# Performance work log

Measured on AMD Instinct MI355X. Metric: run time of the kernel, lower is better.

The kernel has to match this reference:

```python
import jax, jax.numpy as jnp
import numpy as np

B, NA, NT, P, DA, DM, H = 1, 4096, 1024, 32768, 128, 512, 4
DH = DA // H
DF = 4 * DA
WINDOW = 16


def _layer_norm(x, g=None, b=None, eps=1e-5):
    m = jnp.mean(x, axis=-1, keepdims=True)
    v = jnp.var(x, axis=-1, keepdims=True)
    xn = (x - m) / jnp.sqrt(v + eps)
    if g is not None:
        xn = xn * g + b
    return xn


def setup_inputs() -> dict:
    key = jax.random.key(0)
    ks = jax.random.split(key, 32)
    r = lambda k, s: (jax.random.normal(k, s, dtype=jnp.float32) * 0.05)
    return {
        'q': r(ks[0], (B, NA, DA)),
        'c_atom': r(ks[1], (B, NA, DA)),
        'h_cond': r(ks[2], (B, NT, DM)),
        'p_lm': r(ks[3], (B, P, 16)),
        't_emb': r(ks[4], (B, DA)),
        'cond_proj_w': r(ks[5], (DM, DA)), 'cond_proj_b': r(ks[6], (DA,)),
        'adaln1_w': r(ks[7], (DA, 2 * DA)), 'adaln1_b': r(ks[8], (2 * DA,)),
        'adaln2_w': r(ks[9], (DA, 2 * DA)), 'adaln2_b': r(ks[10], (2 * DA,)),
        'ln_g': jnp.ones((DA,), jnp.float32), 'ln_b': jnp.zeros((DA,), jnp.float32),
        'wq': r(ks[11], (DA, DA)), 'wk': r(ks[12], (DA, DA)),
        'wv': r(ks[13], (DA, DA)), 'wg': r(ks[14], (DA, DA)),
        'wo': r(ks[15], (DA, DA)),
        'pair_w': r(ks[16], (16, H)), 'pair_b': r(ks[17], (H,)),
        'gate1_w': r(ks[18], (DA, DA)), 'gate1_b': r(ks[19], (DA,)),
        'gate2_w': r(ks[20], (DA, DA)), 'gate2_b': r(ks[21], (DA,)),
        'sw1': r(ks[22], (DA, DF)), 'sw3': r(ks[23], (DA, DF)),
        'sw2': r(ks[24], (DF, DA)),
        'p_lm_idx': jax.random.randint(ks[25], (B, P, 2), 0, NA, dtype=jnp.int32),
        'token_idx': jnp.sort(jax.random.randint(ks[26], (B, NA), 0, NT, dtype=jnp.int32), axis=-1),
    }


def _forward(q, c_atom, h_cond, p_lm, t_emb,
             cond_proj_w, cond_proj_b, adaln1_w, adaln1_b, adaln2_w, adaln2_b,
             ln_g, ln_b, wq, wk, wv, wg, wo, pair_w, pair_b,
             gate1_w, gate1_b, gate2_w, gate2_b, sw1, sw3, sw2,
             p_lm_idx, token_idx):
    Bq, N, D = q.shape
    # gather token conditioning to atoms: (B, NA, DM)
    h_atoms = jax.vmap(lambda h, t: h[t])(h_cond, token_idx)
    cond = t_emb[:, None, :] + h_atoms @ cond_proj_w + cond_proj_b  # (B, NA, DA)
    g1, b1 = jnp.split(cond @ adaln1_w + adaln1_b, 2, axis=-1)
    q_n = (1.0 + g1) * _layer_norm(q, ln_g, ln_b) + b1

    Q = (q_n @ wq).reshape(Bq, N, H, DH)
    K = (q_n @ wk).reshape(Bq, N, H, DH)
    V = (q_n @ wv).reshape(Bq, N, H, DH)
    G_flat = q_n @ wg  # (B, N, DA); permute/reshape in torch is identity on layout

    scores = jnp.einsum('bihd,bjhd->bhij', Q, K) / jnp.sqrt(jnp.float32(DH))

    # scattered pair bias: (B, P, H) -> dense (B, H, N, N)
    bias = p_lm @ pair_w + pair_b  # (B, P, H)

    def scat(idx, bb):
        return jnp.zeros((N, N, H), bb.dtype).at[idx[:, 0], idx[:, 1]].set(bb)

    pair_bias = jax.vmap(scat)(p_lm_idx, bias).transpose(0, 3, 1, 2)
    scores = scores + pair_bias

    pos = jnp.arange(N)
    window = jnp.abs(pos[:, None] - pos[None, :]) <= WINDOW  # (N, N)
    scores = jnp.where(window[None, None, :, :], scores, -jnp.inf)

    attn = jax.nn.softmax(scores, axis=-1)
    att_out = jnp.einsum('bhij,bjhd->bihd', attn, V).reshape(Bq, N, D)

    q1 = q + jax.nn.sigmoid(G_flat) * (att_out @ wo)
    q1 = q1 + jax.nn.sigmoid(c_atom @ gate1_w + gate1_b) * q1

    g2, b2 = jnp.split(cond @ adaln2_w + adaln2_b, 2, axis=-1)
    q_n2 = (1.0 + g2) * _layer_norm(q1) + b2
    swi = (jax.nn.silu(q_n2 @ sw1) * (q_n2 @ sw3)) @ sw2
    q2 = q1 + jax.nn.sigmoid(c_atom @ gate2_w + gate2_b) * swi
    return q2  # atom_pad_mask is all-ones -> final mask multiply is identity


def reference(q, c_atom, h_cond, p_lm, t_emb,
              cond_proj_w, cond_proj_b, adaln1_w, adaln1_b, adaln2_w, adaln2_b,
              ln_g, ln_b, wq, wk, wv, wg, wo, pair_w, pair_b,
              gate1_w, gate1_b, gate2_w, gate2_b, sw1, sw3, sw2,
              p_lm_idx, token_idx):
    return _forward(q, c_atom, h_cond, p_lm, t_emb,
                    cond_proj_w, cond_proj_b, adaln1_w, adaln1_b, adaln2_w, adaln2_b,
                    ln_g, ln_b, wq, wk, wv, wg, wo, pair_w, pair_b,
                    gate1_w, gate1_b, gate2_w, gate2_b, sw1, sw3, sw2,
                    p_lm_idx, token_idx)
```

## Files before the change

### kernel.cpp

```cpp
#include <hip/hip_runtime.h>
#include <math.h>

#define NA   4096
#define DA   128
#define DM   512
#define NT   1024
#define HH   4
#define DF   512
#define PP   32768
#define WIN  16
#define BAND 33
#define KSTR 132

typedef __attribute__((ext_vector_type(8))) short bf16x8;
typedef __attribute__((ext_vector_type(4))) float f32x4;

__device__ __forceinline__ float sigmoidf_(float x) { return 1.0f / (1.0f + __expf(-x)); }
__device__ __forceinline__ ushort f2bf(float f) {
    union { float f; unsigned int i; } x; x.f = f;
    unsigned int r = x.i + 0x7fffu + ((x.i >> 16) & 1u);
    return (ushort)(r >> 16);
}

__global__ __launch_bounds__(256) void k_prep(
    const float* __restrict__ hc, const float* __restrict__ ca,
    const float* __restrict__ cw, const float* __restrict__ a1, const float* __restrict__ a2,
    const float* __restrict__ wq, const float* __restrict__ wk, const float* __restrict__ wv,
    const float* __restrict__ wg, const float* __restrict__ wo,
    const float* __restrict__ g1, const float* __restrict__ g2,
    const float* __restrict__ s1, const float* __restrict__ s3, const float* __restrict__ s2,
    ushort* hcb, ushort* cab, ushort* cwT, ushort* a1T, ushort* a2T,
    ushort* wqT, ushort* wkT, ushort* wvT, ushort* wgT, ushort* woT,
    ushort* g1T, ushort* g2T, ushort* s1T, ushort* s3T, ushort* s2T,
    float* band)
{
    __shared__ float tile[32][33];
    const int y = blockIdx.y, bx = blockIdx.x, tid = threadIdx.x;
    if (y <= 1) {
        const float4* src = (const float4*)(y == 0 ? hc : ca);
        ushort* dst = y == 0 ? hcb : cab;
        for (int i = bx * 256 + tid; i < 131072; i += 16384) {
            float4 v = src[i];
            ushort4 st; st.x = f2bf(v.x); st.y = f2bf(v.y); st.z = f2bf(v.z); st.w = f2bf(v.w);
            *(ushort4*)&dst[(size_t)i * 4] = st;
        }
        return;
    }
    if (y == 15) {
        float4 z = {0.f, 0.f, 0.f, 0.f};
        float4* b4 = (float4*)band;
        for (int i = bx * 256 + tid; i < 135168; i += 16384) b4[i] = z;
        return;
    }
    const float* src; ushort* dst; int K, N;
    switch (y) {
        case 2:  src = cw; dst = cwT; K = 512; N = 128; break;
        case 3:  src = a1; dst = a1T; K = 128; N = 256; break;
        case 4:  src = a2; dst = a2T; K = 128; N = 256; break;
        case 5:  src = wq; dst = wqT; K = 128; N = 128; break;
        case 6:  src = wk; dst = wkT; K = 128; N = 128; break;
        case 7:  src = wv; dst = wvT; K = 128; N = 128; break;
        case 8:  src = wg; dst = wgT; K = 128; N = 128; break;
        case 9:  src = wo; dst = woT; K = 128; N = 128; break;
        case 10: src = g1; dst = g1T; K = 128; N = 128; break;
        case 11: src = g2; dst = g2T; K = 128; N = 128; break;
        case 12: src = s1; dst = s1T; K = 128; N = 512; break;
        case 13: src = s3; dst = s3T; K = 128; N = 512; break;
        default: src = s2; dst = s2T; K = 512; N = 128; break;
    }
    const int tn_cnt = N >> 5;
    if (bx >= (K >> 5) * tn_cnt) return;
    const int k0 = (bx / tn_cnt) << 5, n0 = (bx % tn_cnt) << 5;
    {
        int r = tid >> 3, c = (tid & 7) << 2;
        float4 v = *(const float4*)&src[(size_t)(k0 + r) * N + n0 + c];
        tile[r][c + 0] = v.x; tile[r][c + 1] = v.y;
        tile[r][c + 2] = v.z; tile[r][c + 3] = v.w;
    }
    __syncthreads();
    {
        int rn = tid >> 3, ck = (tid & 7) << 2;
        ushort4 st;
        st.x = f2bf(tile[ck + 0][rn]);
        st.y = f2bf(tile[ck + 1][rn]);
        st.z = f2bf(tile[ck + 2][rn]);
        st.w = f2bf(tile[ck + 3][rn]);
        *(ushort4*)&dst[(size_t)(n0 + rn) * K + k0 + ck] = st;
    }
}

__global__ __launch_bounds__(256) void k_condmod(
    const ushort* __restrict__ hcb, const int* __restrict__ tok,
    const ushort* __restrict__ cwT, const float* __restrict__ t_emb,
    const float* __restrict__ cond_b, const ushort* __restrict__ cab,
    const ushort* __restrict__ a1T, const ushort* __restrict__ a2T,
    const ushort* __restrict__ g1T, const ushort* __restrict__ g2T,
    const float* __restrict__ ad1b, const float* __restrict__ ad2b,
    const float* __restrict__ g1b, const float* __restrict__ g2b,
    const float* __restrict__ p_lm, const float* __restrict__ pair_w,
    const float* __restrict__ pair_b, const int* __restrict__ p_idx,
    float* __restrict__ band,
    float* __restrict__ gb1, float* __restrict__ gb2,
    float* __restrict__ gate1, float* __restrict__ gate2)
{
    const int tid = threadIdx.x, b = blockIdx.x;
    if (b >= 256) {
        int p = (b - 256) * 256 + tid;
        int i = p_idx[2 * p], j = p_idx[2 * p + 1];
        int d = j - i + WIN;
        if (d < 0 || d > 2 * WIN) return;
        float v0 = pair_b[0], v1 = pair_b[1], v2 = pair_b[2], v3 = pair_b[3];
        #pragma unroll
        for (int k = 0; k < 16; ++k) {
            float a = p_lm[p * 16 + k];
            v0 = fmaf(a, pair_w[k * 4 + 0], v0);
            v1 = fmaf(a, pair_w[k * 4 + 1], v1);
            v2 = fmaf(a, pair_w[k * 4 + 2], v2);
            v3 = fmaf(a, pair_w[k * 4 + 3], v3);
        }
        size_t base = ((size_t)i * HH) * BAND + d;
        band[base + 0 * BAND] = v0;
        band[base + 1 * BAND] = v1;
        band[base + 2 * BAND] = v2;
        band[base + 3 * BAND] = v3;
        return;
    }
    __shared__ ushort cond_s[16 * 128];
    const int l = tid & 63, wv = tid >> 6;
    const int cl = l & 15, kq = l >> 4, ko = kq * 8;
    const int r0 = b * 16;
    {
        const int n0 = wv * 32;
        const ushort* Arow = hcb + (size_t)tok[r0 + cl] * DM;
        const ushort* Wc = cwT + (size_t)(n0 + cl) * DM;
        f32x4 acc[2] = {};
        #pragma unroll
        for (int ks = 0; ks < 16; ++ks) {
            bf16x8 a = *(const bf16x8*)(Arow + ks * 32 + ko);
            #pragma unroll
            for (int nf = 0; nf < 2; ++nf) {
                bf16x8 bb = *(const bf16x8*)(Wc + (size_t)nf * 16 * DM + ks * 32 + ko);
                acc[nf] = __builtin_amdgcn_mfma_f32_16x16x32_bf16(a, bb, acc[nf], 0, 0, 0);
            }
        }
        #pragma unroll
        for (int nf = 0; nf < 2; ++nf) {
            int col = n0 + nf * 16 + cl;
            float add = t_emb[col] + cond_b[col];
            #pragma unroll
            for (int r = 0; r < 4; ++r) {
                int row = kq * 4 + r;
                int byte = row * 256 + col * 2;
                byte ^= (row & 7) << 4;
                *(ushort*)((char*)cond_s + byte) = f2bf(acc[nf][r] + add);
            }
        }
    }
    __syncthreads();
    {
        const int n0 = wv * 64;
        const ushort* W1c = a1T + (size_t)(n0 + cl) * DA;
        const ushort* W2c = a2T + (size_t)(n0 + cl) * DA;
        f32x4 acc1[4] = {}, acc2[4] = {};
        #pragma unroll
        for (int ks = 0; ks < 4; ++ks) {
            int byteA = cl * 256 + (ks * 32 + ko) * 2;
            byteA ^= (cl & 7) << 4;
            bf16x8 a = *(const bf16x8*)((char*)cond_s + byteA);
            #pragma unroll
            for (int nf = 0; nf < 4; ++nf) {
                bf16x8 b1 = *(const bf16x8*)(W1c + (size_t)nf * 16 * DA + ks * 32 + ko);
                acc1[nf] = __builtin_amdgcn_mfma_f32_16x16x32_bf16(a, b1, acc1[nf], 0, 0, 0);
                bf16x8 b2 = *(const bf16x8*)(W2c + (size_t)nf * 16 * DA + ks * 32 + ko);
                acc2[nf] = __builtin_amdgcn_mfma_f32_16x16x32_bf16(a, b2, acc2[nf], 0, 0, 0);
            }
        }
        #pragma unroll
        for (int nf = 0; nf < 4; ++nf) {
            int col = n0 + nf * 16 + cl;
            float b1v = ad1b[col], b2v = ad2b[col];
            #pragma unroll
            for (int r = 0; r < 4; ++r) {
                size_t rc = (size_t)(r0 + kq * 4 + r) * 256 + col;
                gb1[rc] = acc1[nf][r] + b1v;
                gb2[rc] = acc2[nf][r] + b2v;
            }
        }
    }
    {
        const int n0 = wv * 32;
        const ushort* Arow = cab + (size_t)(r0 + cl) * DA;
        const ushort* W1c = g1T + (size_t)(n0 + cl) * DA;
        const ushort* W2c = g2T + (size_t)(n0 + cl) * DA;
        f32x4 acc1[2] = {}, acc2[2] = {};
        #pragma unroll
        for (int ks = 0; ks < 4; ++ks) {
            bf16x8 a = *(const bf16x8*)(Arow + ks * 32 + ko);
            #pragma unroll
            for (int nf = 0; nf < 2; ++nf) {
                bf16x8 b1 = *(const bf16x8*)(W1c + (size_t)nf * 16 * DA + ks * 32 + ko);
                acc1[nf] = __builtin_amdgcn_mfma_f32_16x16x32_bf16(a, b1, acc1[nf], 0, 0, 0);
                bf16x8 b2 = *(const bf16x8*)(W2c + (size_t)nf * 16 * DA + ks * 32 + ko);
                acc2[nf] = __builtin_amdgcn_mfma_f32_16x16x32_bf16(a, b2, acc2[nf], 0, 0, 0);
            }
        }
        #pragma unroll
        for (int nf = 0; nf < 2; ++nf) {
            int col = n0 + nf * 16 + cl;
            float b1v = g1b[col], b2v = g2b[col];
            #pragma unroll
            for (int r = 0; r < 4; ++r) {
                size_t rc = (size_t)(r0 + kq * 4 + r) * DA + col;
                gate1[rc] = sigmoidf_(acc1[nf][r] + b1v);
                gate2[rc] = sigmoidf_(acc2[nf][r] + b2v);
            }
        }
    }
}

__global__ __launch_bounds__(512) void k_mega(
    const float* __restrict__ qg, const float* __restrict__ gb1,
    const float* __restrict__ gb2, const float* __restrict__ gate1,
    const float* __restrict__ gate2, const float* __restrict__ ln_g,
    const float* __restrict__ ln_b, const float* __restrict__ band,
    const ushort* __restrict__ wqT, const ushort* __restrict__ wkT,
    const ushort* __restrict__ wvT, const ushort* __restrict__ wgT,
    const ushort* __restrict__ woT, const ushort* __restrict__ s1T,
    const ushort* __restrict__ s3T, const ushort* __restrict__ s2T,
    float* __restrict__ out)
{
    __shared__ ushort qn_s[48 * 128];
    __shared__ float  K_s[48 * KSTR];
    __shared__ float  V_s[48 * KSTR];
    __shared__ float  Q_s[16 * KSTR];
    __shared__ float  sG_s[16 * KSTR];
    __shared__ float  q1_s[16 * KSTR];
    __shared__ ushort att_s[16 * 128];
    __shared__ ushort hb_s[16 * 512];

    const int tid = threadIdx.x;
    const int l = tid & 63, wv = tid >> 6;
    const int cl = l & 15, kq = l >> 4, ko = kq * 8;
    const int r0 = blockIdx.x * 16;
    const int hb0 = r0 - 16;

    #pragma unroll
    for (int rr = 0; rr < 6; ++rr) {
        int hr = wv * 6 + rr;
        int gr = hb0 + hr;
        ushort2 st = {0, 0};
        if ((unsigned)gr < NA) {
            float2 xv = *(const float2*)&qg[(size_t)gr * DA + 2 * l];
            float sum = xv.x + xv.y, sq = xv.x * xv.x + xv.y * xv.y;
            #pragma unroll
            for (int off = 1; off <= 32; off <<= 1) {
                sum += __shfl_xor(sum, off);
                sq  += __shfl_xor(sq,  off);
            }
            float m = sum * (1.0f / DA);
            float rs = rsqrtf(sq * (1.0f / DA) - m * m + 1e-5f);
            float2 g = *(const float2*)&gb1[(size_t)gr * 256 + 2 * l];
            float2 bb = *(const float2*)&gb1[(size_t)gr * 256 + 128 + 2 * l];
            float2 lg = *(const float2*)&ln_g[2 * l];
            float2 lb = *(const float2*)&ln_b[2 * l];
            float xn0 = (xv.x - m) * rs * lg.x + lb.x;
            float xn1 = (xv.y - m) * rs * lg.y + lb.y;
            st.x = f2bf((1.f + g.x) * xn0 + bb.x);
            st.y = f2bf((1.f + g.y) * xn1 + bb.y);
        }
        int byte = hr * 256 + 4 * l;
        byte ^= (hr & 7) << 4;
        *(ushort2*)((char*)qn_s + byte) = st;
    }
    __syncthreads();

    {
        int t, isV = 0;
        const ushort* WT;
        if (wv < 6) { t = wv >> 1; isV = wv & 1; WT = isV ? wvT : wkT; }
        else        { t = 1; WT = (wv == 6) ? wqT : wgT; }
        const ushort* Wc = WT + (size_t)cl * DA;
        f32x4 acc[8] = {};
        #pragma unroll
        for (int ks = 0; ks < 4; ++ks) {
            int byteA = (t * 16 + cl) * 256 + (ks * 32 + ko) * 2;
            byteA ^= (cl & 7) << 4;
            bf16x8 a = *(const bf16x8*)((char*)qn_s + byteA);
            #pragma unroll
            for (int nf = 0; nf < 8; ++nf) {
                bf16x8 b = *(const bf16x8*)(Wc + (size_t)nf * 16 * DA + ks * 32 + ko);
                acc[nf] = __builtin_amdgcn_mfma_f32_16x16x32_bf16(a, b, acc[nf], 0, 0, 0);
            }
        }
        if (wv < 6) {
            float* dst = isV ? V_s : K_s;
            #pragma unroll
            for (int nf = 0; nf < 8; ++nf)
                #pragma unroll
                for (int r = 0; r < 4; ++r)
                    dst[(t * 16 + kq * 4 + r) * KSTR + nf * 16 + cl] = acc[nf][r];
        } else if (wv == 6) {
            #pragma unroll
            for (int nf = 0; nf < 8; ++nf)
                #pragma unroll
                for (int r = 0; r < 4; ++r)
                    Q_s[(kq * 4 + r) * KSTR + nf * 16 + cl] = acc[nf][r];
        } else {
            #pragma unroll
            for (int nf = 0; nf < 8; ++nf)
                #pragma unroll
                for (int r = 0; r < 4; ++r)
                    sG_s[(kq * 4 + r) * KSTR + nf * 16 + cl] = sigmoidf_(acc[nf][r]);
        }
    }
    __syncthreads();

    {
        const int g = tid >> 3, l3 = tid & 7;
        const int rl = g >> 2, h = g & 3;
        const int gr = r0 + rl;
        const float scale = 0.17677669529663687f;
        float4 qr0 = *(const float4*)&Q_s[rl * KSTR + h * 32 + l3 * 4];
        const float* brow = band + ((size_t)gr * HH + h) * BAND;
        float s[BAND];
        float m = -1e30f;
        #pragma unroll
        for (int jo = 0; jo < BAND; ++jo) {
            int j = gr - WIN + jo;
            float sv = -1e30f;
            if ((unsigned)j < NA) {
                float4 kk = *(const float4*)&K_s[(rl + jo) * KSTR + h * 32 + l3 * 4];
                float d = 0.f;
                d = fmaf(qr0.x, kk.x, d); d = fmaf(qr0.y, kk.y, d);
                d = fmaf(qr0.z, kk.z, d); d = fmaf(qr0.w, kk.w, d);
                d += __shfl_xor(d, 1);
                d += __shfl_xor(d, 2);
                d += __shfl_xor(d, 4);
                sv = fmaf(d, scale, brow[jo]);
            }
            s[jo] = sv;
            m = fmaxf(m, sv);
        }
        float lsum = 0.f;
        #pragma unroll
        for (int jo = 0; jo < BAND; ++jo) {
            float p = __expf(s[jo] - m);
            s[jo] = p;
            lsum += p;
        }
        float inv = 1.0f / lsum;
        float4 o = {0.f, 0.f, 0.f, 0.f};
        #pragma unroll
        for (int jo = 0; jo < BAND; ++jo) {
            int j = gr - WIN + jo;
            if ((unsigned)j < NA) {
                float4 v = *(const float4*)&V_s[(rl + jo) * KSTR + h * 32 + l3 * 4];
                o.x = fmaf(s[jo], v.x, o.x);
                o.y = fmaf(s[jo], v.y, o.y);
                o.z = fmaf(s[jo], v.z, o.z);
                o.w = fmaf(s[jo], v.w, o.w);
            }
        }
        ushort4 st;
        st.x = f2bf(o.x * inv); st.y = f2bf(o.y * inv);
        st.z = f2bf(o.z * inv); st.w = f2bf(o.w * inv);
        int byte = rl * 256 + h * 64 + l3 * 8;
        byte ^= (rl & 7) << 4;
        *(ushort4*)((char*)att_s + byte) = st;
    }
    __syncthreads();

    {
        const int n0 = wv * 16;
        const ushort* Wc = woT + (size_t)(n0 + cl) * DA;
        f32x4 acc = {0.f, 0.f, 0.f, 0.f};
        #pragma unroll
        for (int ks = 0; ks < 4; ++ks) {
            int byteA = cl * 256 + (ks * 32 + ko) * 2;
            byteA ^= (cl & 7) << 4;
            bf16x8 a = *(const bf16x8*)((char*)att_s + byteA);
            bf16x8 b = *(const bf16x8*)(Wc + ks * 32 + ko);
            acc = __builtin_amdgcn_mfma_f32_16x16x32_bf16(a, b, acc, 0, 0, 0);
        }
        #pragma unroll
        for (int r = 0; r < 4; ++r) {
            int row = kq * 4 + r;
            int gr = r0 + row, col = n0 + cl;
            float qv = qg[(size_t)gr * DA + col];
            float sg = sG_s[row * KSTR + col];
            float g1v = gate1[(size_t)gr * DA + col];
            q1_s[row * KSTR + col] = (qv + sg * acc[r]) * (1.f + g1v);
        }
    }
    __syncthreads();

    bf16x8 afr[4];
    {
        const int row = cl, gr = r0 + cl;
        float qv2[4][8];
        float sum = 0.f, sq = 0.f;
        #pragma unroll
        for (int ks = 0; ks < 4; ++ks) {
            float4 v0 = *(const float4*)&q1_s[row * KSTR + ks * 32 + ko];
            float4 v1 = *(const float4*)&q1_s[row * KSTR + ks * 32 + ko + 4];
            qv2[ks][0] = v0.x; qv2[ks][1] = v0.y; qv2[ks][2] = v0.z; qv2[ks][3] = v0.w;
            qv2[ks][4] = v1.x; qv2[ks][5] = v1.y; qv2[ks][6] = v1.z; qv2[ks][7] = v1.w;
            sum += v0.x + v0.y + v0.z + v0.w + v1.x + v1.y + v1.z + v1.w;
            sq += v0.x * v0.x + v0.y * v0.y + v0.z * v0.z + v0.w * v0.w
                + v1.x * v1.x + v1.y * v1.y + v1.z * v1.z + v1.w * v1.w;
        }
        sum += __shfl_xor(sum, 16); sq += __shfl_xor(sq, 16);
        sum += __shfl_xor(sum, 32); sq += __shfl_xor(sq, 32);
        float mean = sum * (1.0f / DA);
        float rs = rsqrtf(sq * (1.0f / DA) - mean * mean + 1e-5f);
        #pragma unroll
        for (int ks = 0; ks < 4; ++ks) {
            int k = ks * 32 + ko;
            float4 g0 = *(const float4*)&gb2[(size_t)gr * 256 + k];
            float4 g1v = *(const float4*)&gb2[(size_t)gr * 256 + k + 4];
            float4 b0 = *(const float4*)&gb2[(size_t)gr * 256 + 128 + k];
            float4 b1v = *(const float4*)&gb2[(size_t)gr * 256 + 128 + k + 4];
            float gg[8] = {g0.x, g0.y, g0.z, g0.w, g1v.x, g1v.y, g1v.z, g1v.w};
            float bb[8] = {b0.x, b0.y, b0.z, b0.w, b1v.x, b1v.y, b1v.z, b1v.w};
            #pragma unroll
            for (int j = 0; j < 8; ++j) {
                float xn = (qv2[ks][j] - mean) * rs;
                afr[ks][j] = (short)f2bf((1.f + gg[j]) * xn + bb[j]);
            }
        }
    }

    {
        const int c0 = wv * 64;
        const ushort* W1 = s1T + (size_t)(c0 + cl) * DA;
        const ushort* W3 = s3T + (size_t)(c0 + cl) * DA;
        f32x4 acc1[4] = {}, acc3[4] = {};
        #pragma unroll
        for (int ks = 0; ks < 4; ++ks) {
            #pragma unroll
            for (int nf = 0; nf < 4; ++nf) {
                bf16x8 b1 = *(const bf16x8*)(W1 + (size_t)nf * 16 * DA + ks * 32 + ko);
                acc1[nf] = __builtin_amdgcn_mfma_f32_16x16x32_bf16(afr[ks], b1, acc1[nf], 0, 0, 0);
                bf16x8 b3 = *(const bf16x8*)(W3 + (size_t)nf * 16 * DA + ks * 32 + ko);
                acc3[nf] = __builtin_amdgcn_mfma_f32_16x16x32_bf16(afr[ks], b3, acc3[nf], 0, 0, 0);
            }
        }
        #pragma unroll
        for (int nf = 0; nf < 4; ++nf) {
            #pragma unroll
            for (int r = 0; r < 4; ++r) {
                float x1 = acc1[nf][r], x3 = acc3[nf][r];
                float h = x1 * sigmoidf_(x1) * x3;
                int rr = kq * 4 + r;
                int col = c0 + nf * 16 + cl;
                int byte = rr * 1024 + col * 2;
                byte ^= (rr & 7) << 4;
                *(ushort*)((char*)hb_s + byte) = f2bf(h);
            }
        }
    }
    __syncthreads();
    {
        const int n0 = wv * 16;
        const ushort* W2 = s2T + (size_t)(n0 + cl) * DF;
        f32x4 acc = {0.f, 0.f, 0.f, 0.f};
        #pragma unroll
        for (int ks = 0; ks < 16; ++ks) {
            int byteA = cl * 1024 + (ks * 32 + ko) * 2;
            byteA ^= (cl & 7) << 4;
            bf16x8 a = *(const bf16x8*)((char*)hb_s + byteA);
            bf16x8 b = *(const bf16x8*)(W2 + ks * 32 + ko);
            acc = __builtin_amdgcn_mfma_f32_16x16x32_bf16(a, b, acc, 0, 0, 0);
        }
        #pragma unroll
        for (int r = 0; r < 4; ++r) {
            int row = kq * 4 + r;
            int gr = r0 + row, col = n0 + cl;
            size_t rc = (size_t)gr * DA + col;
            out[rc] = q1_s[row * KSTR + col] + gate2[rc] * acc[r];
        }
    }
}

extern "C" void kernel_launch(void* const* d_in, const int* in_sizes, int n_in,
                              void* d_out, int out_size, void* d_ws, size_t ws_size,
                              hipStream_t stream)
{
    const float* q      = (const float*)d_in[0];
    const float* c_atom = (const float*)d_in[1];
    const float* h_cond = (const float*)d_in[2];
    const float* p_lm   = (const float*)d_in[3];
    const float* t_emb  = (const float*)d_in[4];
    const float* cond_w = (const float*)d_in[5];
    const float* cond_b = (const float*)d_in[6];
    const float* ad1w   = (const float*)d_in[7];
    const float* ad1b   = (const float*)d_in[8];
    const float* ad2w   = (const float*)d_in[9];
    const float* ad2b   = (const float*)d_in[10];
    const float* ln_g   = (const float*)d_in[11];
    const float* ln_b   = (const float*)d_in[12];
    const float* wq     = (const float*)d_in[13];
    const float* wk     = (const float*)d_in[14];
    const float* wv     = (const float*)d_in[15];
    const float* wg     = (const float*)d_in[16];
    const float* wo     = (const float*)d_in[17];
    const float* pair_w = (const float*)d_in[18];
    const float* pair_b = (const float*)d_in[19];
    const float* g1w    = (const float*)d_in[20];
    const float* g1b    = (const float*)d_in[21];
    const float* g2w    = (const float*)d_in[22];
    const float* g2b    = (const float*)d_in[23];
    const float* sw1    = (const float*)d_in[24];
    const float* sw3    = (const float*)d_in[25];
    const float* sw2    = (const float*)d_in[26];
    const int*   p_idx  = (const int*)d_in[27];
    const int*   tok    = (const int*)d_in[28];
    float* out = (float*)d_out;

    size_t off = 0;
    char* base = (char*)d_ws;
    auto alloc = [&](size_t bytes) -> void* {
        void* p = base + off;
        off += (bytes + 255) & ~(size_t)255;
        return p;
    };
    ushort* hcb     = (ushort*)alloc((size_t)NT * DM * 2);
    ushort* cab     = (ushort*)alloc((size_t)NA * DA * 2);
    ushort* cwT     = (ushort*)alloc((size_t)DM * DA * 2);
    ushort* a1T     = (ushort*)alloc((size_t)256 * 128 * 2);
    ushort* a2T     = (ushort*)alloc((size_t)256 * 128 * 2);
    ushort* wqT     = (ushort*)alloc((size_t)128 * 128 * 2);
    ushort* wkT     = (ushort*)alloc((size_t)128 * 128 * 2);
    ushort* wvT     = (ushort*)alloc((size_t)128 * 128 * 2);
    ushort* wgT     = (ushort*)alloc((size_t)128 * 128 * 2);
    ushort* woT     = (ushort*)alloc((size_t)128 * 128 * 2);
    ushort* g1T     = (ushort*)alloc((size_t)128 * 128 * 2);
    ushort* g2T     = (ushort*)alloc((size_t)128 * 128 * 2);
    ushort* s1T     = (ushort*)alloc((size_t)512 * 128 * 2);
    ushort* s3T     = (ushort*)alloc((size_t)512 * 128 * 2);
    ushort* s2T     = (ushort*)alloc((size_t)128 * 512 * 2);
    float*  gb1     = (float*)alloc((size_t)NA * 256 * 4);
    float*  gb2     = (float*)alloc((size_t)NA * 256 * 4);
    float*  gate1   = (float*)alloc((size_t)NA * DA * 4);
    float*  gate2   = (float*)alloc((size_t)NA * DA * 4);
    float*  band    = (float*)alloc((size_t)NA * HH * BAND * 4);

    k_prep<<<dim3(64, 16), 256, 0, stream>>>(
        h_cond, c_atom, cond_w, ad1w, ad2w, wq, wk, wv, wg, wo,
        g1w, g2w, sw1, sw3, sw2,
        hcb, cab, cwT, a1T, a2T, wqT, wkT, wvT, wgT, woT,
        g1T, g2T, s1T, s3T, s2T, band);
    k_condmod<<<384, 256, 0, stream>>>(
        hcb, tok, cwT, t_emb, cond_b, cab,
        a1T, a2T, g1T, g2T, ad1b, ad2b, g1b, g2b,
        p_lm, pair_w, pair_b, p_idx, band,
        gb1, gb2, gate1, gate2);
    k_mega<<<256, 512, 0, stream>>>(
        q, gb1, gb2, gate1, gate2, ln_g, ln_b, band,
        wqT, wkT, wvT, wgT, woT, s1T, s3T, s2T, out);
    (void)in_sizes; (void)n_in; (void)out_size; (void)ws_size;
}
```

Before: 168.5 us.

## Fuse conditioning, gate and pair-bias computation into the main attention kernel

Removes the separate conditioning kernel and its global intermediates (adaLN scale/shift, sigmoid gates, pair-bias band). The main kernel now computes them per 16-row tile in shared memory: the conditioning GEMM for the 48-row halo, the gate GEMMs, the LayerNorm statistics, and the pair-bias band. The band is built by every block scanning the full pair index list. This cuts a launch and the global round trips. In exchange it recomputes the conditioning for halo rows, repeats the pair scan in every block, and grows shared memory use to about 147KB, which limits occupancy.

Measured after the change: 194.9 us. 1.16x slower.

```diff
diff --git a/kernel.cpp b/kernel.cpp
--- a/kernel.cpp
+++ b/kernel.cpp
@@ -22,6 +22,8 @@
     return (ushort)(r >> 16);
 }
 
+#define MFMA(a, b, c) __builtin_amdgcn_mfma_f32_16x16x32_bf16((a), (b), (c), 0, 0, 0)
+
 __global__ __launch_bounds__(256) void k_prep(
     const float* __restrict__ hc, const float* __restrict__ ca,
     const float* __restrict__ cw, const float* __restrict__ a1, const float* __restrict__ a2,
@@ -31,8 +33,7 @@
     const float* __restrict__ s1, const float* __restrict__ s3, const float* __restrict__ s2,
     ushort* hcb, ushort* cab, ushort* cwT, ushort* a1T, ushort* a2T,
     ushort* wqT, ushort* wkT, ushort* wvT, ushort* wgT, ushort* woT,
-    ushort* g1T, ushort* g2T, ushort* s1T, ushort* s3T, ushort* s2T,
-    float* band)
+    ushort* g1T, ushort* g2T, ushort* s1T, ushort* s3T, ushort* s2T)
 {
     __shared__ float tile[32][33];
     const int y = blockIdx.y, bx = blockIdx.x, tid = threadIdx.x;
@@ -44,12 +45,6 @@
             ushort4 st; st.x = f2bf(v.x); st.y = f2bf(v.y); st.z = f2bf(v.z); st.w = f2bf(v.w);
             *(ushort4*)&dst[(size_t)i * 4] = st;
         }
-        return;
-    }
-    if (y == 15) {
-        float4 z = {0.f, 0.f, 0.f, 0.f};
-        float4* b4 = (float4*)band;
-        for (int i = bx * 256 + tid; i < 135168; i += 16384) b4[i] = z;
         return;
     }
     const float* src; ushort* dst; int K, N;
@@ -89,26 +84,56 @@
     }
 }
 
-__global__ __launch_bounds__(256) void k_condmod(
-    const ushort* __restrict__ hcb, const int* __restrict__ tok,
-    const ushort* __restrict__ cwT, const float* __restrict__ t_emb,
-    const float* __restrict__ cond_b, const ushort* __restrict__ cab,
-    const ushort* __restrict__ a1T, const ushort* __restrict__ a2T,
-    const ushort* __restrict__ g1T, const ushort* __restrict__ g2T,
+__global__ __launch_bounds__(512) void k_mega(
+    const float* __restrict__ qg, const ushort* __restrict__ hcb,
+    const ushort* __restrict__ cab, const int* __restrict__ tok,
+    const float* __restrict__ t_emb, const float* __restrict__ cond_b,
     const float* __restrict__ ad1b, const float* __restrict__ ad2b,
     const float* __restrict__ g1b, const float* __restrict__ g2b,
+    const float* __restrict__ ln_g, const float* __restrict__ ln_b,
     const float* __restrict__ p_lm, const float* __restrict__ pair_w,
     const float* __restrict__ pair_b, const int* __restrict__ p_idx,
-    float* __restrict__ band,
-    float* __restrict__ gb1, float* __restrict__ gb2,
-    float* __restrict__ gate1, float* __restrict__ gate2)
+    const ushort* __restrict__ cwT, const ushort* __restrict__ a1T,
+    const ushort* __restrict__ a2T, const ushort* __restrict__ g1T,
+    const ushort* __restrict__ g2T,
+    const ushort* __restrict__ wqT, const ushort* __restrict__ wkT,
+    const ushort* __restrict__ wvT, const ushort* __restrict__ wgT,
+    const ushort* __restrict__ woT, const ushort* __restrict__ s1T,
+    const ushort* __restrict__ s3T, const ushort* __restrict__ s2T,
+    float* __restrict__ out)
 {
-    const int tid = threadIdx.x, b = blockIdx.x;
-    if (b >= 256) {
-        int p = (b - 256) * 256 + tid;
-        int i = p_idx[2 * p], j = p_idx[2 * p + 1];
-        int d = j - i + WIN;
-        if (d < 0 || d > 2 * WIN) return;
+    __shared__ __align__(16) char pool[147328];
+    float*  K_s     = (float*)(pool + 0);
+    float*  V_s     = (float*)(pool + 25344);
+    char*   qn_c    = pool + 50688;
+    float*  Q_s     = (float*)(pool + 62976);
+    float*  sG_s    = (float*)(pool + 71424);
+    float*  q1_s    = (float*)(pool + 79872);
+    float*  gate1_s = (float*)(pool + 88320);
+    float*  gate2_s = (float*)(pool + 96768);
+    float*  g2g_s   = (float*)(pool + 105216);
+    float*  g2b_s   = (float*)(pool + 113664);
+    float*  mu_s    = (float*)(pool + 122112);
+    float*  rs_s    = (float*)(pool + 122304);
+    char*   cond_c  = pool + 122496;
+    char*   att_c   = pool + 122496;
+    char*   hb_c    = pool + 122496;
+    float*  band_s  = (float*)(pool + 138880);
+
+    const int tid = threadIdx.x;
+    const int l = tid & 63, wv = tid >> 6;
+    const int cl = l & 15, kq = l >> 4, ko = kq * 8;
+    const int r0 = blockIdx.x * 16;
+    const int hb0 = r0 - 16;
+
+    for (int i = tid; i < 16 * HH * BAND; i += 512) band_s[i] = 0.f;
+    __syncthreads();
+
+    for (int p = tid; p < PP; p += 512) {
+        int2 ij = *(const int2*)&p_idx[2 * p];
+        int ri = ij.x - r0;
+        int d = ij.y - ij.x + WIN;
+        if (ri < 0 || ri >= 16 || d < 0 || d > 2 * WIN) continue;
         float v0 = pair_b[0], v1 = pair_b[1], v2 = pair_b[2], v3 = pair_b[3];
         #pragma unroll
         for (int k = 0; k < 16; ++k) {
@@ -118,159 +143,148 @@
             v2 = fmaf(a, pair_w[k * 4 + 2], v2);
             v3 = fmaf(a, pair_w[k * 4 + 3], v3);
         }
-        size_t base = ((size_t)i * HH) * BAND + d;
-        band[base + 0 * BAND] = v0;
-        band[base + 1 * BAND] = v1;
-        band[base + 2 * BAND] = v2;
-        band[base + 3 * BAND] = v3;
-        return;
-    }
-    __shared__ ushort cond_s[16 * 128];
-    const int l = tid & 63, wv = tid >> 6;
-    const int cl = l & 15, kq = l >> 4, ko = kq * 8;
-    const int r0 = b * 16;
-    {
-        const int n0 = wv * 32;
-        const ushort* Arow = hcb + (size_t)tok[r0 + cl] * DM;
+        band_s[ri * 132 + 0 * BAND + d] = v0;
+        band_s[ri * 132 + 1 * BAND + d] = v1;
+        band_s[ri * 132 + 2 * BAND + d] = v2;
+        band_s[ri * 132 + 3 * BAND + d] = v3;
+    }
+
+    if (wv < 6) {
+        const int t = wv >> 1, ch = wv & 1;
+        int gr = hb0 + t * 16 + cl;
+        int grc = gr < 0 ? 0 : (gr >= NA ? NA - 1 : gr);
+        const ushort* Arow = hcb + (size_t)tok[grc] * DM;
+        const int n0 = ch * 64;
         const ushort* Wc = cwT + (size_t)(n0 + cl) * DM;
-        f32x4 acc[2] = {};
+        f32x4 acc[4] = {};
         #pragma unroll
         for (int ks = 0; ks < 16; ++ks) {
             bf16x8 a = *(const bf16x8*)(Arow + ks * 32 + ko);
             #pragma unroll
-            for (int nf = 0; nf < 2; ++nf) {
-                bf16x8 bb = *(const bf16x8*)(Wc + (size_t)nf * 16 * DM + ks * 32 + ko);
-                acc[nf] = __builtin_amdgcn_mfma_f32_16x16x32_bf16(a, bb, acc[nf], 0, 0, 0);
-            }
-        }
-        #pragma unroll
-        for (int nf = 0; nf < 2; ++nf) {
+            for (int nf = 0; nf < 4; ++nf) {
+                bf16x8 b = *(const bf16x8*)(Wc + (size_t)nf * 16 * DM + ks * 32 + ko);
+                acc[nf] = MFMA(a, b, acc[nf]);
+            }
+        }
+        #pragma unroll
+        for (int nf = 0; nf < 4; ++nf) {
             int col = n0 + nf * 16 + cl;
             float add = t_emb[col] + cond_b[col];
             #pragma unroll
             for (int r = 0; r < 4; ++r) {
-                int row = kq * 4 + r;
+                int row = t * 16 + kq * 4 + r;
                 int byte = row * 256 + col * 2;
                 byte ^= (row & 7) << 4;
-                *(ushort*)((char*)cond_s + byte) = f2bf(acc[nf][r] + add);
-            }
-        }
-    }
-    __syncthreads();
-    {
-        const int n0 = wv * 64;
-        const ushort* W1c = a1T + (size_t)(n0 + cl) * DA;
-        const ushort* W2c = a2T + (size_t)(n0 + cl) * DA;
-        f32x4 acc1[4] = {}, acc2[4] = {};
-        #pragma unroll
-        for (int ks = 0; ks < 4; ++ks) {
-            int byteA = cl * 256 + (ks * 32 + ko) * 2;
+                *(ushort*)(cond_c + byte) = f2bf(acc[nf][r] + add);
+            }
+        }
+    } else if (wv == 6) {
+        const ushort* Arow = cab + (size_t)(r0 + cl) * DA;
+        f32x4 acc1[8] = {}, acc2[8] = {};
+        #pragma unroll
+        for (int ks = 0; ks < 4; ++ks) {
+            bf16x8 a = *(const bf16x8*)(Arow + ks * 32 + ko);
+            #pragma unroll
+            for (int nf = 0; nf < 8; ++nf) {
+                bf16x8 b1 = *(const bf16x8*)(g1T + (size_t)(nf * 16 + cl) * DA + ks * 32 + ko);
+                acc1[nf] = MFMA(a, b1, acc1[nf]);
+                bf16x8 b2 = *(const bf16x8*)(g2T + (size_t)(nf * 16 + cl) * DA + ks * 32 + ko);
+                acc2[nf] = MFMA(a, b2, acc2[nf]);
+            }
+        }
+        #pragma unroll
+        for (int nf = 0; nf < 8; ++nf) {
+            int col = nf * 16 + cl;
+            #pragma unroll
+            for (int r = 0; r < 4; ++r) {
+                int row = kq * 4 + r;
+                gate1_s[row * KSTR + col] = sigmoidf_(acc1[nf][r] + g1b[col]);
+                gate2_s[row * KSTR + col] = sigmoidf_(acc2[nf][r] + g2b[col]);
+            }
+        }
+    } else {
+        #pragma unroll
+        for (int rr = 0; rr < 12; ++rr) {
+            int hr = rr * 4 + kq;
+            int gr = hb0 + hr;
+            int grc = gr < 0 ? 0 : (gr >= NA ? NA - 1 : gr);
+            float4 v0 = *(const float4*)&qg[(size_t)grc * DA + cl * 8];
+            float4 v1 = *(const float4*)&qg[(size_t)grc * DA + cl * 8 + 4];
+            float sum = v0.x + v0.y + v0.z + v0.w + v1.x + v1.y + v1.z + v1.w;
+            float sq = v0.x * v0.x + v0.y * v0.y + v0.z * v0.z + v0.w * v0.w
+                     + v1.x * v1.x + v1.y * v1.y + v1.z * v1.z + v1.w * v1.w;
+            sum += __shfl_xor(sum, 1); sq += __shfl_xor(sq, 1);
+            sum += __shfl_xor(sum, 2); sq += __shfl_xor(sq, 2);
+            sum += __shfl_xor(sum, 4); sq += __shfl_xor(sq, 4);
+            sum += __shfl_xor(sum, 8); sq += __shfl_xor(sq, 8);
+            if (cl == 0) {
+                float m = sum * (1.0f / DA);
+                mu_s[hr] = m;
+                rs_s[hr] = rsqrtf(sq * (1.0f / DA) - m * m + 1e-5f);
+            }
+        }
+    }
+    __syncthreads();
+
+    if (wv < 6) {
+        const int t = wv >> 1, ch = wv & 1;
+        const int n0 = ch * 64;
+        f32x4 gacc[4] = {}, bacc[4] = {};
+        #pragma unroll
+        for (int ks = 0; ks < 4; ++ks) {
+            int byteA = (t * 16 + cl) * 256 + (ks * 32 + ko) * 2;
             byteA ^= (cl & 7) << 4;
-            bf16x8 a = *(const bf16x8*)((char*)cond_s + byteA);
+            bf16x8 a = *(const bf16x8*)(cond_c + byteA);
             #pragma unroll
             for (int nf = 0; nf < 4; ++nf) {
-                bf16x8 b1 = *(const bf16x8*)(W1c + (size_t)nf * 16 * DA + ks * 32 + ko);
-                acc1[nf] = __builtin_amdgcn_mfma_f32_16x16x32_bf16(a, b1, acc1[nf], 0, 0, 0);
-                bf16x8 b2 = *(const bf16x8*)(W2c + (size_t)nf * 16 * DA + ks * 32 + ko);
-                acc2[nf] = __builtin_amdgcn_mfma_f32_16x16x32_bf16(a, b2, acc2[nf], 0, 0, 0);
+                bf16x8 bg = *(const bf16x8*)(a1T + (size_t)(n0 + nf * 16 + cl) * DA + ks * 32 + ko);
+                gacc[nf] = MFMA(a, bg, gacc[nf]);
+                bf16x8 bb = *(const bf16x8*)(a1T + (size_t)(128 + n0 + nf * 16 + cl) * DA + ks * 32 + ko);
+                bacc[nf] = MFMA(a, bb, bacc[nf]);
             }
         }
         #pragma unroll
         for (int nf = 0; nf < 4; ++nf) {
             int col = n0 + nf * 16 + cl;
-            float b1v = ad1b[col], b2v = ad2b[col];
+            float lg = ln_g[col], lb = ln_b[col];
+            float b1v = ad1b[col], b2v = ad1b[128 + col];
             #pragma unroll
             for (int r = 0; r < 4; ++r) {
-                size_t rc = (size_t)(r0 + kq * 4 + r) * 256 + col;
-                gb1[rc] = acc1[nf][r] + b1v;
-                gb2[rc] = acc2[nf][r] + b2v;
-            }
-        }
-    }
-    {
-        const int n0 = wv * 32;
-        const ushort* Arow = cab + (size_t)(r0 + cl) * DA;
-        const ushort* W1c = g1T + (size_t)(n0 + cl) * DA;
-        const ushort* W2c = g2T + (size_t)(n0 + cl) * DA;
-        f32x4 acc1[2] = {}, acc2[2] = {};
-        #pragma unroll
-        for (int ks = 0; ks < 4; ++ks) {
-            bf16x8 a = *(const bf16x8*)(Arow + ks * 32 + ko);
-            #pragma unroll
-            for (int nf = 0; nf < 2; ++nf) {
-                bf16x8 b1 = *(const bf16x8*)(W1c + (size_t)nf * 16 * DA + ks * 32 + ko);
-                acc1[nf] = __builtin_amdgcn_mfma_f32_16x16x32_bf16(a, b1, acc1[nf], 0, 0, 0);
-                bf16x8 b2 = *(const bf16x8*)(W2c + (size_t)nf * 16 * DA + ks * 32 + ko);
-                acc2[nf] = __builtin_amdgcn_mfma_f32_16x16x32_bf16(a, b2, acc2[nf], 0, 0, 0);
-            }
-        }
-        #pragma unroll
-        for (int nf = 0; nf < 2; ++nf) {
-            int col = n0 + nf * 16 + cl;
-            float b1v = g1b[col], b2v = g2b[col];
-            #pragma unroll
-            for (int r = 0; r < 4; ++r) {
-                size_t rc = (size_t)(r0 + kq * 4 + r) * DA + col;
-                gate1[rc] = sigmoidf_(acc1[nf][r] + b1v);
-                gate2[rc] = sigmoidf_(acc2[nf][r] + b2v);
-            }
-        }
-    }
-}
-
-__global__ __launch_bounds__(512) void k_mega(
-    const float* __restrict__ qg, const float* __restrict__ gb1,
-    const float* __restrict__ gb2, const float* __restrict__ gate1,
-    const float* __restrict__ gate2, const float* __restrict__ ln_g,
-    const float* __restrict__ ln_b, const float* __restrict__ band,
-    const ushort* __restrict__ wqT, const ushort* __restrict__ wkT,
-    const ushort* __restrict__ wvT, const ushort* __restrict__ wgT,
-    const ushort* __restrict__ woT, const ushort* __restrict__ s1T,
-    const ushort* __restrict__ s3T, const ushort* __restrict__ s2T,
-    float* __restrict__ out)
-{
-    __shared__ ushort qn_s[48 * 128];
-    __shared__ float  K_s[48 * KSTR];
-    __shared__ float  V_s[48 * KSTR];
-    __shared__ float  Q_s[16 * KSTR];
-    __shared__ float  sG_s[16 * KSTR];
-    __shared__ float  q1_s[16 * KSTR];
-    __shared__ ushort att_s[16 * 128];
-    __shared__ ushort hb_s[16 * 512];
-
-    const int tid = threadIdx.x;
-    const int l = tid & 63, wv = tid >> 6;
-    const int cl = l & 15, kq = l >> 4, ko = kq * 8;
-    const int r0 = blockIdx.x * 16;
-    const int hb0 = r0 - 16;
-
-    #pragma unroll
-    for (int rr = 0; rr < 6; ++rr) {
-        int hr = wv * 6 + rr;
-        int gr = hb0 + hr;
-        ushort2 st = {0, 0};
-        if ((unsigned)gr < NA) {
-            float2 xv = *(const float2*)&qg[(size_t)gr * DA + 2 * l];
-            float sum = xv.x + xv.y, sq = xv.x * xv.x + xv.y * xv.y;
-            #pragma unroll
-            for (int off = 1; off <= 32; off <<= 1) {
-                sum += __shfl_xor(sum, off);
-                sq  += __shfl_xor(sq,  off);
-            }
-            float m = sum * (1.0f / DA);
-            float rs = rsqrtf(sq * (1.0f / DA) - m * m + 1e-5f);
-            float2 g = *(const float2*)&gb1[(size_t)gr * 256 + 2 * l];
-            float2 bb = *(const float2*)&gb1[(size_t)gr * 256 + 128 + 2 * l];
-            float2 lg = *(const float2*)&ln_g[2 * l];
-            float2 lb = *(const float2*)&ln_b[2 * l];
-            float xn0 = (xv.x - m) * rs * lg.x + lb.x;
-            float xn1 = (xv.y - m) * rs * lg.y + lb.y;
-            st.x = f2bf((1.f + g.x) * xn0 + bb.x);
-            st.y = f2bf((1.f + g.y) * xn1 + bb.y);
-        }
-        int byte = hr * 256 + 4 * l;
-        byte ^= (hr & 7) << 4;
-        *(ushort2*)((char*)qn_s + byte) = st;
+                int row = t * 16 + kq * 4 + r;
+                int gr = hb0 + row;
+                int grc = gr < 0 ? 0 : (gr >= NA ? NA - 1 : gr);
+                float g = gacc[nf][r] + b1v;
+                float b = bacc[nf][r] + b2v;
+                float qv = qg[(size_t)grc * DA + col];
+                float xn = (qv - mu_s[row]) * rs_s[row] * lg + lb;
+                int byte = row * 256 + col * 2;
+                byte ^= (row & 7) << 4;
+                *(ushort*)(qn_c + byte) = f2bf((1.f + g) * xn + b);
+            }
+        }
+    } else {
+        const int off = (wv == 7) ? 128 : 0;
+        float* dst = (wv == 7) ? g2b_s : g2g_s;
+        f32x4 acc[8] = {};
+        #pragma unroll
+        for (int ks = 0; ks < 4; ++ks) {
+            int byteA = (16 + cl) * 256 + (ks * 32 + ko) * 2;
+            byteA ^= (cl & 7) << 4;
+            bf16x8 a = *(const bf16x8*)(cond_c + byteA);
+            #pragma unroll
+            for (int nf = 0; nf < 8; ++nf) {
+                bf16x8 b = *(const bf16x8*)(a2T + (size_t)(off + nf * 16 + cl) * DA + ks * 32 + ko);
+                acc[nf] = MFMA(a, b, acc[nf]);
+            }
+        }
+        #pragma unroll
+        for (int nf = 0; nf < 8; ++nf) {
+            int col = nf * 16 + cl;
+            float bb = ad2b[off + col];
+            #pragma unroll
+            for (int r = 0; r < 4; ++r)
+                dst[(kq * 4 + r) * KSTR + col] = acc[nf][r] + bb;
+        }
     }
     __syncthreads();
 
@@ -285,11 +299,11 @@
         for (int ks = 0; ks < 4; ++ks) {
             int byteA = (t * 16 + cl) * 256 + (ks * 32 + ko) * 2;
             byteA ^= (cl & 7) << 4;
-            bf16x8 a = *(const bf16x8*)((char*)qn_s + byteA);
+            bf16x8 a = *(const bf16x8*)(qn_c + byteA);
             #pragma unroll
             for (int nf = 0; nf < 8; ++nf) {
                 bf16x8 b = *(const bf16x8*)(Wc + (size_t)nf * 16 * DA + ks * 32 + ko);
-                acc[nf] = __builtin_amdgcn_mfma_f32_16x16x32_bf16(a, b, acc[nf], 0, 0, 0);
+                acc[nf] = MFMA(a, b, acc[nf]);
             }
         }
         if (wv < 6) {
@@ -321,7 +335,7 @@
         const int gr = r0 + rl;
         const float scale = 0.17677669529663687f;
         float4 qr0 = *(const float4*)&Q_s[rl * KSTR + h * 32 + l3 * 4];
-        const float* brow = band + ((size_t)gr * HH + h) * BAND;
+        const float* brow = band_s + rl * 132 + h * BAND;
         float s[BAND];
         float m = -1e30f;
         #pragma unroll
@@ -366,7 +380,7 @@
         st.z = f2bf(o.z * inv); st.w = f2bf(o.w * inv);
         int byte = rl * 256 + h * 64 + l3 * 8;
         byte ^= (rl & 7) << 4;
-        *(ushort4*)((char*)att_s + byte) = st;
+        *(ushort4*)(att_c + byte) = st;
     }
     __syncthreads();
 
@@ -378,9 +392,9 @@
         for (int ks = 0; ks < 4; ++ks) {
             int byteA = cl * 256 + (ks * 32 + ko) * 2;
             byteA ^= (cl & 7) << 4;
-            bf16x8 a = *(const bf16x8*)((char*)att_s + byteA);
+            bf16x8 a = *(const bf16x8*)(att_c + byteA);
             bf16x8 b = *(const bf16x8*)(Wc + ks * 32 + ko);
-            acc = __builtin_amdgcn_mfma_f32_16x16x32_bf16(a, b, acc, 0, 0, 0);
+            acc = MFMA(a, b, acc);
         }
         #pragma unroll
         for (int r = 0; r < 4; ++r) {
@@ -388,7 +402,7 @@
             int gr = r0 + row, col = n0 + cl;
             float qv = qg[(size_t)gr * DA + col];
             float sg = sG_s[row * KSTR + col];
-            float g1v = gate1[(size_t)gr * DA + col];
+            float g1v = gate1_s[row * KSTR + col];
             q1_s[row * KSTR + col] = (qv + sg * acc[r]) * (1.f + g1v);
         }
     }
@@ -396,7 +410,7 @@
 
     bf16x8 afr[4];
     {
-        const int row = cl, gr = r0 + cl;
+        const int row = cl;
         float qv2[4][8];
         float sum = 0.f, sq = 0.f;
         #pragma unroll
@@ -416,10 +430,10 @@
         #pragma unroll
         for (int ks = 0; ks < 4; ++ks) {
             int k = ks * 32 + ko;
-            float4 g0 = *(const float4*)&gb2[(size_t)gr * 256 + k];
-            float4 g1v = *(const float4*)&gb2[(size_t)gr * 256 + k + 4];
-            float4 b0 = *(const float4*)&gb2[(size_t)gr * 256 + 128 + k];
-            float4 b1v = *(const float4*)&gb2[(size_t)gr * 256 + 128 + k + 4];
+            float4 g0 = *(const float4*)&g2g_s[row * KSTR + k];
+            float4 g1v = *(const float4*)&g2g_s[row * KSTR + k + 4];
+            float4 b0 = *(const float4*)&g2b_s[row * KSTR + k];
+            float4 b1v = *(const float4*)&g2b_s[row * KSTR + k + 4];
             float gg[8] = {g0.x, g0.y, g0.z, g0.w, g1v.x, g1v.y, g1v.z, g1v.w};
             float bb[8] = {b0.x, b0.y, b0.z, b0.w, b1v.x, b1v.y, b1v.z, b1v.w};
             #pragma unroll
@@ -440,11 +454,12 @@
             #pragma unroll
             for (int nf = 0; nf < 4; ++nf) {
                 bf16x8 b1 = *(const bf16x8*)(W1 + (size_t)nf * 16 * DA + ks * 32 + ko);
-                acc1[nf] = __builtin_amdgcn_mfma_f32_16x16x32_bf16(afr[ks], b1, acc1[nf], 0, 0, 0);
+                acc1[nf] = MFMA(afr[ks], b1, acc1[nf]);
                 bf16x8 b3 = *(const bf16x8*)(W3 + (size_t)nf * 16 * DA + ks * 32 + ko);
-                acc3[nf] = __builtin_amdgcn_mfma_f32_16x16x32_bf16(afr[ks], b3, acc3[nf], 0, 0, 0);
-            }
-        }
+                acc3[nf] = MFMA(afr[ks], b3, acc3[nf]);
+            }
+        }
+        __syncthreads();
         #pragma unroll
         for (int nf = 0; nf < 4; ++nf) {
             #pragma unroll
@@ -455,7 +470,7 @@
                 int col = c0 + nf * 16 + cl;
                 int byte = rr * 1024 + col * 2;
                 byte ^= (rr & 7) << 4;
-                *(ushort*)((char*)hb_s + byte) = f2bf(h);
+                *(ushort*)(hb_c + byte) = f2bf(h);
             }
         }
     }
@@ -468,16 +483,16 @@
         for (int ks = 0; ks < 16; ++ks) {
             int byteA = cl * 1024 + (ks * 32 + ko) * 2;
             byteA ^= (cl & 7) << 4;
-            bf16x8 a = *(const bf16x8*)((char*)hb_s + byteA);
+            bf16x8 a = *(const bf16x8*)(hb_c + byteA);
             bf16x8 b = *(const bf16x8*)(W2 + ks * 32 + ko);
-            acc = __builtin_amdgcn_mfma_f32_16x16x32_bf16(a, b, acc, 0, 0, 0);
+            acc = MFMA(a, b, acc);
         }
         #pragma unroll
         for (int r = 0; r < 4; ++r) {
             int row = kq * 4 + r;
             int gr = r0 + row, col = n0 + cl;
             size_t rc = (size_t)gr * DA + col;
-            out[rc] = q1_s[row * KSTR + col] + gate2[rc] * acc[r];
+            out[rc] = q1_s[row * KSTR + col] + gate2_s[row * KSTR + col] * acc[r];
         }
     }
 }
@@ -524,39 +539,31 @@
         off += (bytes + 255) & ~(size_t)255;
         return p;
     };
-    ushort* hcb     = (ushort*)alloc((size_t)NT * DM * 2);
-    ushort* cab     = (ushort*)alloc((size_t)NA * DA * 2);
-    ushort* cwT     = (ushort*)alloc((size_t)DM * DA * 2);
-    ushort* a1T     = (ushort*)alloc((size_t)256 * 128 * 2);
-    ushort* a2T     = (ushort*)alloc((size_t)256 * 128 * 2);
-    ushort* wqT     = (ushort*)alloc((size_t)128 * 128 * 2);
-    ushort* wkT     = (ushort*)alloc((size_t)128 * 128 * 2);
-    ushort* wvT     = (ushort*)alloc((size_t)128 * 128 * 2);
-    ushort* wgT     = (ushort*)alloc((size_t)128 * 128 * 2);
-    ushort* woT     = (ushort*)alloc((size_t)128 * 128 * 2);
-    ushort* g1T     = (ushort*)alloc((size_t)128 * 128 * 2);
-    ushort* g2T     = (ushort*)alloc((size_t)128 * 128 * 2);
-    ushort* s1T     = (ushort*)alloc((size_t)512 * 128 * 2);
-    ushort* s3T     = (ushort*)alloc((size_t)512 * 128 * 2);
-    ushort* s2T     = (ushort*)alloc((size_t)128 * 512 * 2);
-    float*  gb1     = (float*)alloc((size_t)NA * 256 * 4);
-    float*  gb2     = (float*)alloc((size_t)NA * 256 * 4);
-    float*  gate1   = (float*)alloc((size_t)NA * DA * 4);
-    float*  gate2   = (float*)alloc((size_t)NA * DA * 4);
-    float*  band    = (float*)alloc((size_t)NA * HH * BAND * 4);
-
-    k_prep<<<dim3(64, 16), 256, 0, stream>>>(
+    ushort* hcb = (ushort*)alloc((size_t)NT * DM * 2);
+    ushort* cab = (ushort*)alloc((size_t)NA * DA * 2);
+    ushort* cwT = (ushort*)alloc((size_t)DM * DA * 2);
+    ushort* a1T = (ushort*)alloc((size_t)256 * 128 * 2);
+    ushort* a2T = (ushort*)alloc((size_t)256 * 128 * 2);
+    ushort* wqT = (ushort*)alloc((size_t)128 * 128 * 2);
+    ushort* wkT = (ushort*)alloc((size_t)128 * 128 * 2);
+    ushort* wvT = (ushort*)alloc((size_t)128 * 128 * 2);
+    ushort* wgT = (ushort*)alloc((size_t)128 * 128 * 2);
+    ushort* woT = (ushort*)alloc((size_t)128 * 128 * 2);
+    ushort* g1T = (ushort*)alloc((size_t)128 * 128 * 2);
+    ushort* g2T = (ushort*)alloc((size_t)128 * 128 * 2);
+    ushort* s1T = (ushort*)alloc((size_t)512 * 128 * 2);
+    ushort* s3T = (ushort*)alloc((size_t)512 * 128 * 2);
+    ushort* s2T = (ushort*)alloc((size_t)128 * 512 * 2);
+
+    k_prep<<<dim3(64, 15), 256, 0, stream>>>(
         h_cond, c_atom, cond_w, ad1w, ad2w, wq, wk, wv, wg, wo,
         g1w, g2w, sw1, sw3, sw2,
         hcb, cab, cwT, a1T, a2T, wqT, wkT, wvT, wgT, woT,
-        g1T, g2T, s1T, s3T, s2T, band);
-    k_condmod<<<384, 256, 0, stream>>>(
-        hcb, tok, cwT, t_emb, cond_b, cab,
-        a1T, a2T, g1T, g2T, ad1b, ad2b, g1b, g2b,
-        p_lm, pair_w, pair_b, p_idx, band,
-        gb1, gb2, gate1, gate2);
+        g1T, g2T, s1T, s3T, s2T);
     k_mega<<<256, 512, 0, stream>>>(
-        q, gb1, gb2, gate1, gate2, ln_g, ln_b, band,
+        q, hcb, cab, tok, t_emb, cond_b, ad1b, ad2b, g1b, g2b,
+        ln_g, ln_b, p_lm, pair_w, pair_b, p_idx,
+        cwT, a1T, a2T, g1T, g2T,
         wqT, wkT, wvT, wgT, woT, s1T, s3T, s2T, out);
     (void)in_sizes; (void)n_in; (void)out_size; (void)ws_size;
 }
```
